# Kernel optimization log

Hardware: AMD Instinct MI355X
Metric: run time of the kernel (lower is better)

The kernel has to match this reference:

```python
import jax, jax.numpy as jnp
import numpy as np

N = 50000        # nodes
E = 1_600_000    # edges (avg degree 32)
IN, HID, OUT = 128, 64, 16


def setup_inputs() -> dict:
    key = jax.random.key(0)
    k0, k1, k2, k3, k4 = jax.random.split(key, 5)
    src = jax.random.randint(k0, (E,), 0, N, dtype=jnp.int32)
    dst = jax.random.randint(k1, (E,), 0, N, dtype=jnp.int32)
    features = jax.random.normal(k2, (N, IN), dtype=jnp.float32)
    W1 = jax.random.normal(k3, (IN, HID), dtype=jnp.float32) / np.float32(np.sqrt(IN))
    b1 = jnp.zeros((HID,), jnp.float32)
    W2 = jax.random.normal(k4, (HID, OUT), dtype=jnp.float32) / np.float32(np.sqrt(HID))
    b2 = jnp.zeros((OUT,), jnp.float32)
    return {"features": features, "W1": W1, "b1": b1, "W2": W2, "b2": b2,
            "src": src, "dst": dst}


def _graph_conv(src, dst, x, W, b):
    # DGL GraphConv, norm='both':  out = D_dst^{-1/2} * A^T * (D_src^{-1/2} * x) @ W + b
    ones = jnp.ones((src.shape[0],), x.dtype)
    deg_out = jax.ops.segment_sum(ones, src, num_segments=N)  # out-degree of source nodes
    deg_in = jax.ops.segment_sum(ones, dst, num_segments=N)   # in-degree of dest nodes
    norm_s = jax.lax.rsqrt(jnp.maximum(deg_out, 1.0))
    norm_d = jax.lax.rsqrt(jnp.maximum(deg_in, 1.0))
    # project first (in_feats >= out_feats) so messages are in the smaller dim
    h = (x * norm_s[:, None]) @ W                              # [N, out_dim]
    agg = jax.ops.segment_sum(h[src], dst, num_segments=N)     # sparse aggregate
    return agg * norm_d[:, None] + b


def reference(features, W1, b1, W2, b2, src, dst):
    h = jax.nn.relu(_graph_conv(src, dst, features, W1, b1))
    return _graph_conv(src, dst, h, W2, b2)
```

## Files before the change

### kernel.cpp

```cpp
#include <hip/hip_runtime.h>
#include <hip/hip_fp16.h>

#define IN_F  128
#define HID_F 64
#define OUT_F 16
#define MAX_N 50176
#define HWORDS (MAX_N / 2)
#define QWORDS (MAX_N / 4)
#define NSEG  256

#define SCAN_CHUNK 1024

#define LSTR 136
#define XSTR 68

typedef __attribute__((ext_vector_type(8))) _Float16 half8;
typedef __attribute__((ext_vector_type(4))) _Float16 half4v;
typedef __attribute__((ext_vector_type(4))) float    floatx4;

__global__ __launch_bounds__(1024) void hist2_kernel(const int* __restrict__ src,
                                                     const int* __restrict__ dst,
                                                     unsigned int* __restrict__ partial,
                                                     int E, int seg, int Wr8) {
    __shared__ unsigned int cnt[QWORDS];
    int b = blockIdx.x;
    const int* ids = blockIdx.y ? dst : src;
    unsigned int* pbase = partial + (size_t)blockIdx.y * NSEG * Wr8;
    for (int w = threadIdx.x; w < Wr8; w += 1024) cnt[w] = 0;
    __syncthreads();
    int lo = b * seg, hi = min(lo + seg, E);
    for (int e = lo + threadIdx.x; e < hi; e += 1024) {
        int d = ids[e];
        atomicAdd(&cnt[d >> 2], 1u << ((d & 3) * 8));
    }
    __syncthreads();
    for (int w = threadIdx.x; w < Wr8; w += 1024)
        pbase[(size_t)b * Wr8 + w] = cnt[w];
}

__global__ __launch_bounds__(256) void reduce_norm2_kernel(unsigned int* __restrict__ partial,
                                                           unsigned int* __restrict__ wsum,
                                                           float* __restrict__ norm_s,
                                                           float* __restrict__ norm_d,
                                                           int Wr8, int N) {
    int wave = threadIdx.x >> 6, lane = threadIdx.x & 63;
    int p = blockIdx.x * 4 + wave;
    int w0 = 2 * p;
    if (w0 >= Wr8) return;
    bool pair = (w0 + 1 < Wr8);

    if (blockIdx.y == 0) {
        const unsigned int* base = partial;
        unsigned int s0 = 0, s1 = 0;
        #pragma unroll
        for (int j = 0; j < 4; j++) {
            size_t idx = (size_t)(4 * lane + j) * Wr8 + w0;
            if (pair) { uint2 v = *(const uint2*)(base + idx); s0 += v.x; s1 += v.y; }
            else      { s0 += base[idx]; }
        }
        #pragma unroll
        for (int off = 1; off < 64; off <<= 1) {
            s0 += __shfl_xor(s0, off);
            s1 += __shfl_xor(s1, off);
        }
        if (lane == 0) {
            int d = 4 * w0;
            if (d     < N) norm_s[d]     = rsqrtf(fmaxf((float)( s0        & 0xFFu), 1.0f));
            if (d + 1 < N) norm_s[d + 1] = rsqrtf(fmaxf((float)((s0 >>  8) & 0xFFu), 1.0f));
            if (d + 2 < N) norm_s[d + 2] = rsqrtf(fmaxf((float)((s0 >> 16) & 0xFFu), 1.0f));
            if (d + 3 < N) norm_s[d + 3] = rsqrtf(fmaxf((float)( s0 >> 24        ), 1.0f));
            if (pair) {
                if (d + 4 < N) norm_s[d + 4] = rsqrtf(fmaxf((float)( s1        & 0xFFu), 1.0f));
                if (d + 5 < N) norm_s[d + 5] = rsqrtf(fmaxf((float)((s1 >>  8) & 0xFFu), 1.0f));
                if (d + 6 < N) norm_s[d + 6] = rsqrtf(fmaxf((float)((s1 >> 16) & 0xFFu), 1.0f));
                if (d + 7 < N) norm_s[d + 7] = rsqrtf(fmaxf((float)( s1 >> 24        ), 1.0f));
            }
        }
        return;
    }

    unsigned int* base = partial + (size_t)NSEG * Wr8;
    unsigned int a0[4], a1[4];
    #pragma unroll
    for (int j = 0; j < 4; j++) {
        size_t idx = (size_t)(4 * lane + j) * Wr8 + w0;
        if (pair) { uint2 v = *(const uint2*)(base + idx); a0[j] = v.x; a1[j] = v.y; }
        else      { a0[j] = base[idx]; a1[j] = 0u; }
    }
    unsigned int e0[4], e1[4], l0 = 0, l1 = 0;
    #pragma unroll
    for (int j = 0; j < 4; j++) {
        e0[j] = l0; l0 += a0[j];
        e1[j] = l1; l1 += a1[j];
    }
    unsigned int inc0 = l0, inc1 = l1;
    #pragma unroll
    for (int off = 1; off < 64; off <<= 1) {
        unsigned int v0 = __shfl_up(inc0, off);
        unsigned int v1 = __shfl_up(inc1, off);
        if (lane >= off) { inc0 += v0; inc1 += v1; }
    }
    unsigned int exc0 = __shfl_up(inc0, 1);
    unsigned int exc1 = __shfl_up(inc1, 1);
    if (lane == 0) { exc0 = 0; exc1 = 0; }
    #pragma unroll
    for (int j = 0; j < 4; j++) {
        size_t idx = (size_t)(4 * lane + j) * Wr8 + w0;
        if (pair) { uint2 v; v.x = exc0 + e0[j]; v.y = exc1 + e1[j]; *(uint2*)(base + idx) = v; }
        else      { base[idx] = exc0 + e0[j]; }
    }
    unsigned int tot0 = __shfl(inc0, 63);
    unsigned int tot1 = __shfl(inc1, 63);
    if (lane == 0) {
        wsum[w0] = tot0;
        if (pair) wsum[w0 + 1] = tot1;
        int d = 4 * w0;
        if (d     < N) norm_d[d]     = rsqrtf(fmaxf((float)( tot0        & 0xFFu), 1.0f));
        if (d + 1 < N) norm_d[d + 1] = rsqrtf(fmaxf((float)((tot0 >>  8) & 0xFFu), 1.0f));
        if (d + 2 < N) norm_d[d + 2] = rsqrtf(fmaxf((float)((tot0 >> 16) & 0xFFu), 1.0f));
        if (d + 3 < N) norm_d[d + 3] = rsqrtf(fmaxf((float)( tot0 >> 24        ), 1.0f));
        if (pair) {
            if (d + 4 < N) norm_d[d + 4] = rsqrtf(fmaxf((float)( tot1        & 0xFFu), 1.0f));
            if (d + 5 < N) norm_d[d + 5] = rsqrtf(fmaxf((float)((tot1 >>  8) & 0xFFu), 1.0f));
            if (d + 6 < N) norm_d[d + 6] = rsqrtf(fmaxf((float)((tot1 >> 16) & 0xFFu), 1.0f));
            if (d + 7 < N) norm_d[d + 7] = rsqrtf(fmaxf((float)( tot1 >> 24        ), 1.0f));
        }
    }
}

__global__ __launch_bounds__(256) void scan_local_kernel(const unsigned int* __restrict__ wsum,
                                                         int* __restrict__ row_start,
                                                         int* __restrict__ bsum,
                                                         int Wr8, int N) {
    __shared__ int wsums[4];
    int t = threadIdx.x;
    int wave = t >> 6, lane = t & 63;
    int w = blockIdx.x * 256 + t;
    unsigned int v = (w < Wr8) ? wsum[w] : 0u;
    int c0 = (int)(v & 0xFFu), c1 = (int)((v >> 8) & 0xFFu);
    int c2 = (int)((v >> 16) & 0xFFu), c3 = (int)(v >> 24);
    int s = c0 + c1 + c2 + c3;
    int inc = s;
    #pragma unroll
    for (int off = 1; off < 64; off <<= 1) {
        int x = __shfl_up(inc, off);
        if (lane >= off) inc += x;
    }
    if (lane == 63) wsums[wave] = inc;
    __syncthreads();
    int woff = 0;
    #pragma unroll
    for (int k = 0; k < 4; k++) woff += (k < wave) ? wsums[k] : 0;
    int run = woff + inc - s;
    int d = 4 * w;
    if (d     < N) row_start[d]     = run;
    run += c0;
    if (d + 1 < N) row_start[d + 1] = run;
    run += c1;
    if (d + 2 < N) row_start[d + 2] = run;
    run += c2;
    if (d + 3 < N) row_start[d + 3] = run;
    if (t == 0) bsum[blockIdx.x] = wsums[0] + wsums[1] + wsums[2] + wsums[3];
}

__global__ __launch_bounds__(1024) void scan_bsum_kernel(int* __restrict__ bsum, int nblocks) {
    __shared__ int part[1024];
    int t = threadIdx.x;
    int v = (t < nblocks) ? bsum[t] : 0;
    part[t] = v;
    __syncthreads();
    for (int off = 1; off < 1024; off <<= 1) {
        int x = (t >= off) ? part[t - off] : 0;
        __syncthreads();
        part[t] += x;
        __syncthreads();
    }
    if (t < nblocks) bsum[t] = part[t] - v;
}

__global__ __launch_bounds__(1024) void scatter_lds_kernel(const int* __restrict__ src,
                                                           const int* __restrict__ dst,
                                                           const int* __restrict__ row_start,
                                                           const int* __restrict__ bsum,
                                                           const unsigned int* __restrict__ prefix,
                                                           unsigned short* __restrict__ csr_src,
                                                           int E, int seg, int Wr8, int N,
                                                           int nchunks) {
    __shared__ unsigned int pos[HWORDS];
    __shared__ int sbsum[64];
    int b = blockIdx.x;
    int t = threadIdx.x;
    if (t < 64) sbsum[t] = (t < nchunks) ? bsum[t] : 0;
    int half = (N + 1) >> 1;
    for (int w = t; w < half; w += 1024) {
        int d0 = 2 * w, d1 = 2 * w + 1;
        unsigned int word = prefix[(size_t)b * Wr8 + (w >> 1)];
        unsigned int b0 = (word >> ((d0 & 3) * 8)) & 0xFFu;
        unsigned int b1 = (word >> ((d1 & 3) * 8)) & 0xFFu;
        unsigned int lo = (unsigned int)row_start[d0] + b0;
        unsigned int hi = (d1 < N) ? ((unsigned int)row_start[d1] + b1) : 0u;
        pos[w] = lo | (hi << 16);
    }
    __syncthreads();
    int lo = b * seg, hiE = min(lo + seg, E);
    for (int e = lo + t; e < hiE; e += 1024) {
        int d = dst[e];
        unsigned int sh = (unsigned int)(d & 1) * 16u;
        unsigned int old = atomicAdd(&pos[d >> 1], 1u << sh);
        unsigned int q = (old >> sh) & 0xFFFFu;
        csr_src[q + (unsigned int)sbsum[d >> 10]] = (unsigned short)src[e];
    }
}

__global__ __launch_bounds__(256) void gemm1_kernel(const float* __restrict__ x,
                                                    const float* __restrict__ W,
                                                    const float* __restrict__ norm_s,
                                                    __half* __restrict__ h, int N) {
    __shared__ _Float16 sx[64 * LSTR];
    __shared__ _Float16 sw[64 * LSTR];
    int t = threadIdx.x;
    int row0 = blockIdx.x * 64;

    for (int i = t; i < IN_F * 16; i += 256) {
        int k = i >> 4, n4 = (i & 15) * 4;
        float4 w4 = *(const float4*)(W + (size_t)k * HID_F + n4);
        sw[(n4 + 0) * LSTR + k] = (_Float16)w4.x;
        sw[(n4 + 1) * LSTR + k] = (_Float16)w4.y;
        sw[(n4 + 2) * LSTR + k] = (_Float16)w4.z;
        sw[(n4 + 3) * LSTR + k] = (_Float16)w4.w;
    }
    for (int i = t; i < 64 * 32; i += 256) {
        int r = i >> 5, k4 = (i & 31) * 4;
        int gr = row0 + r;
        half4v hv = {0, 0, 0, 0};
        if (gr < N) {
            float4 v = *(const float4*)(x + (size_t)gr * IN_F + k4);
            float ns = norm_s[gr];
            hv.x = (_Float16)(v.x * ns); hv.y = (_Float16)(v.y * ns);
            hv.z = (_Float16)(v.z * ns); hv.w = (_Float16)(v.w * ns);
        }
        *(half4v*)(sx + r * LSTR + k4) = hv;
    }
    __syncthreads();

    int wave = t >> 6, lane = t & 63;
    int m = lane & 15, quad = lane >> 4;
    int rbase = wave * 16;

    floatx4 acc[4] = {{0,0,0,0}, {0,0,0,0}, {0,0,0,0}, {0,0,0,0}};
    #pragma unroll
    for (int ks = 0; ks < 4; ks++) {
        half8 av = *(half8*)(sx + (rbase + m) * LSTR + ks * 32 + quad * 8);
        #pragma unroll
        for (int ct = 0; ct < 4; ct++) {
            half8 bv = *(half8*)(sw + (ct * 16 + m) * LSTR + ks * 32 + quad * 8);
            acc[ct] = __builtin_amdgcn_mfma_f32_16x16x32_f16(av, bv, acc[ct], 0, 0, 0);
        }
    }
    #pragma unroll
    for (int ct = 0; ct < 4; ct++) {
        #pragma unroll
        for (int reg = 0; reg < 4; reg++) {
            int gr = row0 + rbase + quad * 4 + reg;
            if (gr < N) h[(size_t)gr * HID_F + ct * 16 + m] = __float2half(acc[ct][reg]);
        }
    }
}

__global__ __launch_bounds__(256) void agg1_kernel(const int* __restrict__ row_start,
                                                   const int* __restrict__ bsum,
                                                   const unsigned short* __restrict__ csr_src,
                                                   const __half* __restrict__ h,
                                                   const float* __restrict__ norm_d,
                                                   const float* __restrict__ norm_s,
                                                   const float* __restrict__ b1,
                                                   const float* __restrict__ W2,
                                                   __half* __restrict__ h2, int N, int E) {
    __shared__ float sW2T[OUT_F][XSTR];
    __shared__ float xrow[16][XSTR];
    int t = threadIdx.x;
    for (int i = t; i < HID_F * OUT_F; i += 256) {
        int k = i >> 4, o = i & 15;
        sW2T[o][k] = W2[i];
    }

    int wave = t >> 6, lane = t & 63;
    int slot = lane >> 3;
    int fh   = lane & 7;
    int nbase = blockIdx.x * 16 + wave * 4;

    int rs[5];
    #pragma unroll
    for (int j = 0; j < 5; j++) {
        int n = nbase + j;
        rs[j] = (n < N) ? (row_start[n] + bsum[n >> 10]) : E;
    }

    #pragma unroll
    for (int nn = 0; nn < 4; nn++) {
        int node = nbase + nn;
        if (node < N) {
            int beg = rs[nn], end = rs[nn + 1];

            float f[8] = {0.f, 0.f, 0.f, 0.f, 0.f, 0.f, 0.f, 0.f};

            #define AGG1_BODY(SIDX) {                                                  \
                const uint4* p = (const uint4*)(h + (size_t)(SIDX) * HID_F + fh * 8);  \
                uint4 u = *p;                                                          \
                __half2 q0 = *(__half2*)&u.x, q1 = *(__half2*)&u.y;                    \
                __half2 q2 = *(__half2*)&u.z, q3 = *(__half2*)&u.w;                    \
                float2 g0 = __half22float2(q0), g1 = __half22float2(q1);               \
                float2 g2 = __half22float2(q2), g3 = __half22float2(q3);               \
                f[0] += g0.x; f[1] += g0.y; f[2] += g1.x; f[3] += g1.y;                \
                f[4] += g2.x; f[5] += g2.y; f[6] += g3.x; f[7] += g3.y; }

            int i = beg + slot;
            for (; i + 24 < end; i += 32) {
                int s0 = (int)csr_src[i];
                int s1 = (int)csr_src[i + 8];
                int s2 = (int)csr_src[i + 16];
                int s3 = (int)csr_src[i + 24];
                AGG1_BODY(s0); AGG1_BODY(s1); AGG1_BODY(s2); AGG1_BODY(s3);
            }
            for (; i < end; i += 8) {
                int s = (int)csr_src[i];
                AGG1_BODY(s);
            }
            #undef AGG1_BODY

            #pragma unroll
            for (int j = 0; j < 8; j++) {
                f[j] += __shfl_xor(f[j], 8);
                f[j] += __shfl_xor(f[j], 16);
                f[j] += __shfl_xor(f[j], 32);
            }

            if (slot == 0) {
                float nd = norm_d[node], ns = norm_s[node];
                const float4 bA = *(const float4*)(b1 + fh * 8);
                const float4 bB = *(const float4*)(b1 + fh * 8 + 4);
                float4 vA, vB;
                vA.x = fmaxf(f[0] * nd + bA.x, 0.f) * ns;
                vA.y = fmaxf(f[1] * nd + bA.y, 0.f) * ns;
                vA.z = fmaxf(f[2] * nd + bA.z, 0.f) * ns;
                vA.w = fmaxf(f[3] * nd + bA.w, 0.f) * ns;
                vB.x = fmaxf(f[4] * nd + bB.x, 0.f) * ns;
                vB.y = fmaxf(f[5] * nd + bB.y, 0.f) * ns;
                vB.z = fmaxf(f[6] * nd + bB.z, 0.f) * ns;
                vB.w = fmaxf(f[7] * nd + bB.w, 0.f) * ns;
                *(float4*)&xrow[wave * 4 + nn][fh * 8]     = vA;
                *(float4*)&xrow[wave * 4 + nn][fh * 8 + 4] = vB;
            }
        }
    }
    __syncthreads();

    int nr = t >> 4, o = t & 15;
    int gnode = blockIdx.x * 16 + nr;
    if (gnode < N) {
        float acc = 0.0f;
        #pragma unroll
        for (int k4 = 0; k4 < HID_F / 4; k4++) {
            float4 x4 = *(const float4*)&xrow[nr][k4 * 4];
            float4 w4 = *(const float4*)&sW2T[o][k4 * 4];
            acc += x4.x * w4.x + x4.y * w4.y + x4.z * w4.z + x4.w * w4.w;
        }
        h2[(size_t)gnode * OUT_F + o] = __float2half(acc);
    }
}

__global__ __launch_bounds__(256) void agg2_kernel(const int* __restrict__ row_start,
                                                   const int* __restrict__ bsum,
                                                   const unsigned short* __restrict__ csr_src,
                                                   const __half* __restrict__ h2,
                                                   const float* __restrict__ norm_d,
                                                   const float* __restrict__ b2,
                                                   float* __restrict__ out, int N, int E) {
    int node = blockIdx.x * 4 + (threadIdx.x >> 6);
    if (node >= N) return;
    int lane = threadIdx.x & 63;
    int slot = lane >> 2;
    int fh   = lane & 3;
    int beg = row_start[node] + bsum[node >> 10];
    int end = (node + 1 < N) ? row_start[node + 1] + bsum[(node + 1) >> 10] : E;

    float f0 = 0.f, f1 = 0.f, f2 = 0.f, f3 = 0.f;

    #define AGG2_BODY(SIDX) {                                                  \
        const uint2* p = (const uint2*)(h2 + (size_t)(SIDX) * OUT_F + fh * 4); \
        uint2 u = *p;                                                          \
        __half2 q0 = *(__half2*)&u.x, q1 = *(__half2*)&u.y;                    \
        float2 g0 = __half22float2(q0), g1 = __half22float2(q1);               \
        f0 += g0.x; f1 += g0.y; f2 += g1.x; f3 += g1.y; }

    int i = beg + slot;
    for (; i + 16 < end; i += 32) {
        int s0 = (int)csr_src[i];
        int s1 = (int)csr_src[i + 16];
        AGG2_BODY(s0); AGG2_BODY(s1);
    }
    if (i < end) {
        int s = (int)csr_src[i];
        AGG2_BODY(s);
    }
    #undef AGG2_BODY

    f0 += __shfl_xor(f0, 4);  f1 += __shfl_xor(f1, 4);
    f2 += __shfl_xor(f2, 4);  f3 += __shfl_xor(f3, 4);
    f0 += __shfl_xor(f0, 8);  f1 += __shfl_xor(f1, 8);
    f2 += __shfl_xor(f2, 8);  f3 += __shfl_xor(f3, 8);
    f0 += __shfl_xor(f0, 16); f1 += __shfl_xor(f1, 16);
    f2 += __shfl_xor(f2, 16); f3 += __shfl_xor(f3, 16);
    f0 += __shfl_xor(f0, 32); f1 += __shfl_xor(f1, 32);
    f2 += __shfl_xor(f2, 32); f3 += __shfl_xor(f3, 32);

    if (slot == 0) {
        float nd = norm_d[node];
        float4 v;
        v.x = f0 * nd + b2[fh * 4 + 0];
        v.y = f1 * nd + b2[fh * 4 + 1];
        v.z = f2 * nd + b2[fh * 4 + 2];
        v.w = f3 * nd + b2[fh * 4 + 3];
        *(float4*)(out + (size_t)node * OUT_F + fh * 4) = v;
    }
}

extern "C" void kernel_launch(void* const* d_in, const int* in_sizes, int n_in,
                              void* d_out, int out_size, void* d_ws, size_t ws_size,
                              hipStream_t stream) {
    const float* feat = (const float*)d_in[0];
    const float* W1   = (const float*)d_in[1];
    const float* b1   = (const float*)d_in[2];
    const float* W2   = (const float*)d_in[3];
    const float* b2   = (const float*)d_in[4];
    const int*   src  = (const int*)d_in[5];
    const int*   dst  = (const int*)d_in[6];

    const int N   = in_sizes[0] / IN_F;
    const int E   = in_sizes[5];
    const int seg = (E + NSEG - 1) / NSEG;
    const int Wr8 = (N + 3) >> 2;
    const int nchunks = (N + SCAN_CHUNK - 1) / SCAN_CHUNK;
    const int npairs  = (Wr8 + 1) >> 1;

    float* fws    = (float*)d_ws;
    float* norm_s = fws;
    float* norm_d = fws + N;
    __half* h1    = (__half*)(fws + 2 * (size_t)N);
    __half* h2    = h1 + (size_t)N * HID_F;
    int*   iws    = (int*)(h2 + (size_t)N * OUT_F);
    int*   row_start = iws;
    int*   bsum      = iws + N + 1;
    unsigned int* wsum = (unsigned int*)(iws + N + 1 + 1024);
    unsigned int* partial = wsum + Wr8;
    unsigned short* csr_src = (unsigned short*)(partial + 2 * (size_t)NSEG * Wr8);

    hist2_kernel<<<dim3(NSEG, 2), 1024, 0, stream>>>(src, dst, partial, E, seg, Wr8);
    reduce_norm2_kernel<<<dim3((npairs + 3) / 4, 2), 256, 0, stream>>>(partial, wsum, norm_s, norm_d, Wr8, N);
    scan_local_kernel<<<nchunks, 256, 0, stream>>>(wsum, row_start, bsum, Wr8, N);
    scan_bsum_kernel<<<1, 1024, 0, stream>>>(bsum, nchunks);

    scatter_lds_kernel<<<NSEG, 1024, 0, stream>>>(src, dst, row_start, bsum,
                                                  partial + (size_t)NSEG * Wr8,
                                                  csr_src, E, seg, Wr8, N, nchunks);

    gemm1_kernel<<<(N + 63) / 64, 256, 0, stream>>>(feat, W1, norm_s, h1, N);
    agg1_kernel<<<(N + 15) / 16, 256, 0, stream>>>(row_start, bsum, csr_src, h1, norm_d, norm_s, b1, W2, h2, N, E);
    agg2_kernel<<<(N + 3) / 4, 256, 0, stream>>>(row_start, bsum, csr_src, h2, norm_d, b2, (float*)d_out, N, E);
}
```

Baseline: 223.7 us.

## Halve edge segments and scatter with 32-bit LDS cursors over node passes

Cuts the number of edge segments from 256 to 128, so the histogram and partial-prefix arrays shrink and each reduce lane handles two segments instead of four. The scatter kernel no longer packs two 16-bit cursors per LDS word. It keeps one 32-bit absolute cursor per node and splits the node range into passes over blockIdx.y, each pass handling the edges whose destination falls in that half. This removes the packed-atomic shift/mask and the separate per-chunk offset table. In exchange, every block reads its edge segment once per pass, segments are larger so fewer blocks run the histogram, and the 8-bit per-segment counters hold more edges each, which raises overflow risk on skewed graphs.

```diff
diff --git a/kernel.cpp b/kernel.cpp
--- a/kernel.cpp
+++ b/kernel.cpp
@@ -7,7 +7,7 @@
 #define MAX_N 50176
 #define HWORDS (MAX_N / 2)
 #define QWORDS (MAX_N / 4)
-#define NSEG  256
+#define NSEG  128
 
 #define SCAN_CHUNK 1024
 
@@ -53,8 +53,8 @@
         const unsigned int* base = partial;
         unsigned int s0 = 0, s1 = 0;
         #pragma unroll
-        for (int j = 0; j < 4; j++) {
-            size_t idx = (size_t)(4 * lane + j) * Wr8 + w0;
+        for (int j = 0; j < 2; j++) {
+            size_t idx = (size_t)(2 * lane + j) * Wr8 + w0;
             if (pair) { uint2 v = *(const uint2*)(base + idx); s0 += v.x; s1 += v.y; }
             else      { s0 += base[idx]; }
         }
@@ -80,16 +80,16 @@
     }
 
     unsigned int* base = partial + (size_t)NSEG * Wr8;
-    unsigned int a0[4], a1[4];
-    #pragma unroll
-    for (int j = 0; j < 4; j++) {
-        size_t idx = (size_t)(4 * lane + j) * Wr8 + w0;
+    unsigned int a0[2], a1[2];
+    #pragma unroll
+    for (int j = 0; j < 2; j++) {
+        size_t idx = (size_t)(2 * lane + j) * Wr8 + w0;
         if (pair) { uint2 v = *(const uint2*)(base + idx); a0[j] = v.x; a1[j] = v.y; }
         else      { a0[j] = base[idx]; a1[j] = 0u; }
     }
-    unsigned int e0[4], e1[4], l0 = 0, l1 = 0;
-    #pragma unroll
-    for (int j = 0; j < 4; j++) {
+    unsigned int e0[2], e1[2], l0 = 0, l1 = 0;
+    #pragma unroll
+    for (int j = 0; j < 2; j++) {
         e0[j] = l0; l0 += a0[j];
         e1[j] = l1; l1 += a1[j];
     }
@@ -104,8 +104,8 @@
     unsigned int exc1 = __shfl_up(inc1, 1);
     if (lane == 0) { exc0 = 0; exc1 = 0; }
     #pragma unroll
-    for (int j = 0; j < 4; j++) {
-        size_t idx = (size_t)(4 * lane + j) * Wr8 + w0;
+    for (int j = 0; j < 2; j++) {
+        size_t idx = (size_t)(2 * lane + j) * Wr8 + w0;
         if (pair) { uint2 v; v.x = exc0 + e0[j]; v.y = exc1 + e1[j]; *(uint2*)(base + idx) = v; }
         else      { base[idx] = exc0 + e0[j]; }
     }
@@ -184,31 +184,24 @@
                                                            const int* __restrict__ bsum,
                                                            const unsigned int* __restrict__ prefix,
                                                            unsigned short* __restrict__ csr_src,
-                                                           int E, int seg, int Wr8, int N,
-                                                           int nchunks) {
+                                                           int E, int seg, int Wr8, int N) {
     __shared__ unsigned int pos[HWORDS];
-    __shared__ int sbsum[64];
     int b = blockIdx.x;
-    int t = threadIdx.x;
-    if (t < 64) sbsum[t] = (t < nchunks) ? bsum[t] : 0;
-    int half = (N + 1) >> 1;
-    for (int w = t; w < half; w += 1024) {
-        int d0 = 2 * w, d1 = 2 * w + 1;
-        unsigned int word = prefix[(size_t)b * Wr8 + (w >> 1)];
-        unsigned int b0 = (word >> ((d0 & 3) * 8)) & 0xFFu;
-        unsigned int b1 = (word >> ((d1 & 3) * 8)) & 0xFFu;
-        unsigned int lo = (unsigned int)row_start[d0] + b0;
-        unsigned int hi = (d1 < N) ? ((unsigned int)row_start[d1] + b1) : 0u;
-        pos[w] = lo | (hi << 16);
-    }
-    __syncthreads();
-    int lo = b * seg, hiE = min(lo + seg, E);
-    for (int e = lo + t; e < hiE; e += 1024) {
+    int p = blockIdx.y;
+    int lo = b * seg, hi = min(lo + seg, E);
+    int nlo = p * HWORDS, nhi = min(nlo + HWORDS, N);
+    for (int d = nlo + threadIdx.x; d < nhi; d += 1024) {
+        unsigned int word = prefix[(size_t)b * Wr8 + (d >> 2)];
+        unsigned int base8 = (word >> ((d & 3) * 8)) & 0xFFu;
+        pos[d - nlo] = (unsigned int)(row_start[d] + bsum[d >> 10]) + base8;
+    }
+    __syncthreads();
+    for (int e = lo + threadIdx.x; e < hi; e += 1024) {
         int d = dst[e];
-        unsigned int sh = (unsigned int)(d & 1) * 16u;
-        unsigned int old = atomicAdd(&pos[d >> 1], 1u << sh);
-        unsigned int q = (old >> sh) & 0xFFFFu;
-        csr_src[q + (unsigned int)sbsum[d >> 10]] = (unsigned short)src[e];
+        if (d >= nlo && d < nhi) {
+            unsigned int q = atomicAdd(&pos[d - nlo], 1u);
+            csr_src[q] = (unsigned short)src[e];
+        }
     }
 }
 
@@ -441,6 +434,7 @@
     const int seg = (E + NSEG - 1) / NSEG;
     const int Wr8 = (N + 3) >> 2;
     const int nchunks = (N + SCAN_CHUNK - 1) / SCAN_CHUNK;
+    const int npass   = (N + HWORDS - 1) / HWORDS;
     const int npairs  = (Wr8 + 1) >> 1;
 
     float* fws    = (float*)d_ws;
@@ -460,9 +454,9 @@
     scan_local_kernel<<<nchunks, 256, 0, stream>>>(wsum, row_start, bsum, Wr8, N);
     scan_bsum_kernel<<<1, 1024, 0, stream>>>(bsum, nchunks);
 
-    scatter_lds_kernel<<<NSEG, 1024, 0, stream>>>(src, dst, row_start, bsum,
-                                                  partial + (size_t)NSEG * Wr8,
-                                                  csr_src, E, seg, Wr8, N, nchunks);
+    scatter_lds_kernel<<<dim3(NSEG, npass), 1024, 0, stream>>>(src, dst, row_start, bsum,
+                                                               partial + (size_t)NSEG * Wr8,
+                                                               csr_src, E, seg, Wr8, N);
 
     gemm1_kernel<<<(N + 63) / 64, 256, 0, stream>>>(feat, W1, norm_s, h1, N);
     agg1_kernel<<<(N + 15) / 16, 256, 0, stream>>>(row_start, bsum, csr_src, h1, norm_d, norm_s, b1, W2, h2, N, E);
```

After: 201.9 us (median of 2 runs). 9.8% less time.
